# Kernel optimization log

Measured on AMD Instinct MI355X. Metric: run time of the kernel, lower is better.

Reference implementation:

```python
import jax, jax.numpy as jnp
import numpy as np

K_EDE = 10.0   # self.k
T_EDE = 0.1    # self.t
BN_EPS = 1e-5
T_A = 576.0    # 3*3*64, hardcoded in my_bn1/my_bn2


def qfn(x, prec):
    # dorefa-style round quantizer with straight-through gradient
    n = float(2 ** prec - 1)
    return x + jax.lax.stop_gradient(jnp.round(x * n) / n - x)


@jax.custom_vjp
def binary_quantize(x):
    return jnp.sign(x)


def _bq_fwd(x):
    return jnp.sign(x), x


def _bq_bwd(x, g):
    # IR-Net EDE backward: k * t * (1 - tanh(x*t)^2)
    return (K_EDE * T_EDE * (1.0 - jnp.tanh(x * T_EDE) ** 2) * g,)


binary_quantize.defvjp(_bq_fwd, _bq_bwd)


def _clip_T(x):
    T = jnp.maximum(jnp.abs(x.min()), jnp.abs(x.max()))
    return jax.lax.stop_gradient(jnp.clip(T, 1e-10, 255.0))


def quantize_conv_act(x, prec):
    # my_quantize_conv: clamp to [-T, T], scale to [-1,1], qfn (no rescale by T)
    T = _clip_T(x)
    return qfn(jnp.clip(x, -T, T) / T, prec)


def quantize(x, prec):
    # my_quantize: same but rescaled back by T
    T = _clip_T(x)
    return qfn(jnp.clip(x, -T, T) / T, prec) * T


def ir_conv2d(a, w, stride):
    # IR-Net 1w8a IRConv2d: per-out-channel normalize, binarize (sign), power-of-2 scale
    co = w.shape[0]
    wf = w.reshape(co, -1)
    bw = (w - wf.mean(1)[:, None, None, None]) / jnp.std(wf, axis=1, ddof=1)[:, None, None, None]
    sw = jax.lax.stop_gradient(
        2.0 ** jnp.round(jnp.log2(jnp.abs(bw.reshape(co, -1)).mean(1)))
    )[:, None, None, None]
    bw = binary_quantize(bw) * sw
    return jax.lax.conv_general_dilated(
        a, bw, window_strides=(stride, stride), padding=[(1, 1), (1, 1)],
        dimension_numbers=('NCHW', 'OIHW', 'NCHW'))


def bn_as_quantized_affine(x, gamma, beta, mean, var):
    # my_bn1/my_bn2 (eval mode): BN folded into per-channel scale+bias.
    # The original builds a CxC diagonal 1x1 conv; since off-diagonal entries are 0,
    # both the quantization stats (max|.|) and the conv reduce exactly to this
    # per-channel affine, which is the faithful fused form.
    std = jnp.sqrt(var + BN_EPS)
    w = gamma / std
    b = beta - w * mean
    qw = quantize(w, 3)
    qb = quantize(b, 12)
    aq = qfn(x / T_A, 10) * T_A  # my_quantize_activation(input, 10, T_a)
    return aq * qw[None, :, None, None] + qb[None, :, None, None]


def _block(x, w1, w2, g1, b1, m1, v1, g2, b2, m2, v2):
    xq = quantize_conv_act(x, 3)
    out = ir_conv2d(xq, w1, 1)
    out = bn_as_quantized_affine(out, g1, b1, m1, v1) + xq  # identity shortcut
    out = jnp.clip(out, -1.0, 1.0)  # hardtanh
    x1 = quantize_conv_act(out, 3)
    out = ir_conv2d(x1, w2, 1)
    out = bn_as_quantized_affine(out, g2, b2, m2, v2) + x1
    return jnp.clip(out, -1.0, 1.0)


def setup_inputs() -> dict:
    key = jax.random.key(0)
    ks = jax.random.split(key, 11)
    B, C, H, W = 128, 64, 56, 56
    return {
        'x': jax.random.normal(ks[0], (B, C, H, W), jnp.float32),
        'w1': jax.random.normal(ks[1], (C, C, 3, 3), jnp.float32) * 0.1,
        'w2': jax.random.normal(ks[2], (C, C, 3, 3), jnp.float32) * 0.1,
        'g1': jax.random.uniform(ks[3], (C,), jnp.float32, 0.5, 1.5),
        'b1': jax.random.normal(ks[4], (C,), jnp.float32) * 0.1,
        'm1': jax.random.normal(ks[5], (C,), jnp.float32) * 0.1,
        'v1': jax.random.uniform(ks[6], (C,), jnp.float32, 0.5, 1.5),
        'g2': jax.random.uniform(ks[7], (C,), jnp.float32, 0.5, 1.5),
        'b2': jax.random.normal(ks[8], (C,), jnp.float32) * 0.1,
        'm2': jax.random.normal(ks[9], (C,), jnp.float32) * 0.1,
        'v2': jax.random.uniform(ks[10], (C,), jnp.float32, 0.5, 1.5),
    }


def reference(x, w1, w2, g1, b1, m1, v1, g2, b2, m2, v2):
    return _block(x, w1, w2, g1, b1, m1, v1, g2, b2, m2, v2)
```

## Files before the change

kernel.cpp:

```cpp
#include <hip/hip_runtime.h>
#include <stdint.h>

typedef int v4i   __attribute__((ext_vector_type(4)));
typedef int v16i  __attribute__((ext_vector_type(16)));

#define B_    128
#define C_    64
#define H_    56
#define W_    56
#define HW_   3136
#define NELEM (B_*C_*HW_)

#define OFF_K0   0
#define OFF_K1   ((size_t)NELEM)
#define OFF_WB   ((size_t)2*NELEM)
#define OFF_PAR  (OFF_WB + 2*4*9*64*16)
#define OFF_MAX  (OFF_PAR + 384*4)

__device__ __forceinline__ float pw_reduce64(float r) {
    r = __fadd_rn(r, __shfl_xor(r, 1, 64));
    r = __fadd_rn(r, __shfl_xor(r, 2, 64));
    r = __fadd_rn(r, __shfl_xor(r, 4, 64));
    r = __fadd_rn(r, __shfl_xor(r, 8, 64));
    r = __fadd_rn(r, __shfl_xor(r, 16, 64));
    r = __fadd_rn(r, __shfl_xor(r, 32, 64));
    return r;
}

__global__ void k_pre(const float* __restrict__ x, unsigned* __restrict__ maxbits,
                      const float* __restrict__ w1, const float* __restrict__ w2,
                      int8_t* __restrict__ wb, float* __restrict__ par,
                      const float* __restrict__ g1, const float* __restrict__ bb1,
                      const float* __restrict__ mm1, const float* __restrict__ vv1,
                      const float* __restrict__ g2, const float* __restrict__ bb2,
                      const float* __restrict__ mm2, const float* __restrict__ vv2) {
    __shared__ float smax[4];
    const int b = blockIdx.x;
    const int tid = threadIdx.x;
    if (b < 1024) {
        float m = 0.f;
        const int n4 = NELEM / 4;
        for (int i = b * 256 + tid; i < n4; i += 1024 * 256) {
            float4 v = ((const float4*)x)[i];
            m = fmaxf(m, fmaxf(fmaxf(fabsf(v.x), fabsf(v.y)), fmaxf(fabsf(v.z), fabsf(v.w))));
        }
        for (int off = 32; off; off >>= 1) m = fmaxf(m, __shfl_down(m, off, 64));
        if ((tid & 63) == 0) smax[tid >> 6] = m;
        __syncthreads();
        if (tid == 0) {
            float mm = fmaxf(fmaxf(smax[0], smax[1]), fmaxf(smax[2], smax[3]));
            atomicMax(maxbits, __float_as_uint(mm));
        }
    } else if (b < 1056) {
        const int idx = (b - 1024) * 4 + (tid >> 6);
        const int layer = idx >> 6, co = idx & 63;
        const int lane = tid & 63;
        const float* w = (layer ? w2 : w1) + (size_t)co * 576;
        const int base = (lane >> 3) * 72 + (lane & 7);

        float v[9];
#pragma unroll
        for (int i = 0; i < 9; i++) v[i] = w[base + 8 * i];

        float s = v[0];
#pragma unroll
        for (int i = 1; i < 9; i++) s = __fadd_rn(s, v[i]);
        const float mean = __fdiv_rn(pw_reduce64(s), 576.0f);

        float d0 = __fsub_rn(v[0], mean);
        float sq = __fmul_rn(d0, d0);
#pragma unroll
        for (int i = 1; i < 9; i++) {
            float d = __fsub_rn(v[i], mean);
            sq = __fadd_rn(sq, __fmul_rn(d, d));
        }
        const float sig = __fsqrt_rn(__fdiv_rn(pw_reduce64(sq), 575.0f));

        float sa = fabsf(__fdiv_rn(__fsub_rn(v[0], mean), sig));
#pragma unroll
        for (int i = 1; i < 9; i++)
            sa = __fadd_rn(sa, fabsf(__fdiv_rn(__fsub_rn(v[i], mean), sig)));
        const float ma = __fdiv_rn(pw_reduce64(sa), 576.0f);
        const float p  = rintf(log2f(ma));
        if (lane == 0) par[256 + layer * 64 + co] = __fdiv_rn(exp2f(p), 7.0f);

#pragma unroll
        for (int i = 0; i < 9; i++) {
            int ig = base + 8 * i;
            float d = __fsub_rn(v[i], mean);
            int8_t sg = (d > 0.0f) ? (int8_t)1 : ((d < 0.0f) ? (int8_t)-1 : (int8_t)0);
            int ci = ig / 9, tp = ig % 9;
            wb[((((size_t)layer * 4 + (ci >> 4)) * 9 + tp) * 64 + co) * 16 + (ci & 15)] = sg;
        }
    } else {
        if (tid < 128) {
            const int layer = tid >> 6;
            const int c = tid & 63;
            const float* g  = layer ? g2  : g1;
            const float* be = layer ? bb2 : bb1;
            const float* mu = layer ? mm2 : mm1;
            const float* va = layer ? vv2 : vv1;
            const float stdv = __fsqrt_rn(__fadd_rn(va[c], 1e-5f));
            const float w = __fdiv_rn(g[c], stdv);
            const float bb = __fsub_rn(be[c], __fmul_rn(w, mu[c]));
            float aw = fabsf(w), ab = fabsf(bb);
            for (int off = 32; off; off >>= 1) {
                aw = fmaxf(aw, __shfl_xor(aw, off, 64));
                ab = fmaxf(ab, __shfl_xor(ab, off, 64));
            }
            const float Tw = fminf(fmaxf(aw, 1e-10f), 255.0f);
            const float Tb = fminf(fmaxf(ab, 1e-10f), 255.0f);
            {
                float vq = __fdiv_rn(fminf(fmaxf(w, -Tw), Tw), Tw);
                float r  = rintf(__fmul_rn(vq, 7.0f));
                float qf = __fadd_rn(vq, __fsub_rn(__fdiv_rn(r, 7.0f), vq));
                par[layer * 64 + c] = __fmul_rn(qf, Tw);
            }
            {
                float vq = __fdiv_rn(fminf(fmaxf(bb, -Tb), Tb), Tb);
                float r  = rintf(__fmul_rn(vq, 4095.0f));
                float qf = __fadd_rn(vq, __fsub_rn(__fdiv_rn(r, 4095.0f), vq));
                par[128 + layer * 64 + c] = __fmul_rn(qf, Tb);
            }
        }
    }
}

__global__ void k_quant(const float* __restrict__ x, const unsigned* __restrict__ maxbits,
                        int8_t* __restrict__ k8) {
    __shared__ unsigned tile[56 * 17];
    const int n = blockIdx.x / H_;
    const int y = blockIdx.x % H_;
    const float T = fminf(fmaxf(__uint_as_float(*maxbits), 1e-10f), 255.0f);
    const double dinv = 1.0 / (double)T;
    const int t = threadIdx.x;
    if (t < 224) {
        const int cb = t / 14, xb = t % 14;
        const float* src = x + ((size_t)(n * 64 + 4 * cb)) * HW_ + y * 56 + 4 * xb;
        int kq[4][4];
#pragma unroll
        for (int i = 0; i < 4; i++) {
            float4 v = *(const float4*)(src + (size_t)i * HW_);
            const float e[4] = {v.x, v.y, v.z, v.w};
#pragma unroll
            for (int j = 0; j < 4; j++) {
                const float tc = fminf(fmaxf(e[j], -T), T);
                const float u  = (float)((double)tc * dinv);
                kq[i][j] = (int)rintf(__fmul_rn(u, 7.0f));
            }
        }
#pragma unroll
        for (int j = 0; j < 4; j++) {
            const unsigned d = (kq[0][j] & 255) | ((kq[1][j] & 255) << 8) |
                               ((kq[2][j] & 255) << 16) | ((unsigned)(kq[3][j] & 255) << 24);
            tile[(4 * xb + j) * 17 + cb] = d;
        }
    }
    __syncthreads();
    unsigned* dst = (unsigned*)(k8 + ((size_t)(n * 56 + y)) * 56 * 64);
    for (int u = t; u < 896; u += 256)
        dst[u] = tile[(u >> 4) * 17 + (u & 15)];
}

#define EPI_CHAIN(S_, scf_, kc_, qwf_, qbf_, OUT_)                          \
    {   const float Sf_ = (float)(S_);                                      \
        const float convf_ = __fmul_rn(Sf_, scf_);                          \
        const float xb_ = (float)((double)convf_ * (1.0 / 576.0));          \
        const float rr_ = rintf(__fmul_rn(xb_, 1023.0f));                   \
        const float q1_ = (float)((double)rr_ * (1.0 / 1023.0));            \
        const float y1_ = __fadd_rn(xb_, __fsub_rn(q1_, xb_));              \
        const float aq_ = __fmul_rn(y1_, 576.0f);                           \
        const float xqv_ = (float)((double)(kc_) * (1.0 / 7.0));            \
        float vv_ = __fadd_rn(__fadd_rn(__fmul_rn(aq_, qwf_), qbf_), xqv_); \
        OUT_ = fminf(fmaxf(vv_, -1.0f), 1.0f); }

__global__ __launch_bounds__(448, 2) void k_fused(const int8_t* __restrict__ k0,
                                                  const int8_t* __restrict__ wb,
                                                  const float* __restrict__ par,
                                                  float* __restrict__ fout) {
    __shared__ __align__(16) int8_t wsm[2 * 4 * 9 * 64 * 16];
    __shared__ __align__(16) int8_t k0b[4 * 8 * 58 * 16];
    __shared__ __align__(16) int8_t x1b[4 * 8 * 58 * 16];
    const int n = blockIdx.x >> 1;
    const int b = (blockIdx.x & 1) * 28;
    const int tid = threadIdx.x;
    const int wv = tid >> 6, lane = tid & 63;
    const int mbase = wv * 32;
    const int ml = lane & 31;
    const int khalf = lane >> 5;
    const int m = mbase + ml;
    const int ym = m / 56, cm = m % 56;

    for (int u = tid; u < 4608; u += 448)
        *(int4*)(wsm + u * 16) = *(const int4*)(wb + (size_t)u * 16);
    for (int u = tid; u < 1392; u += 448) {
        const int q = u & 3, vv = u >> 2;
        const int rr = vv / 58, xp = vv % 58;
        const int r = b - 2 + rr, xg = xp - 1;
        int4 val = {0, 0, 0, 0};
        if (r >= 0 && r < 56 && xg >= 0 && xg < 56)
            val = *(const int4*)(k0 + (((size_t)(n * 56 + r)) * 56 + xg) * 64 + q * 16);
        *(int4*)(k0b + (((q * 8 + ((r + 2) & 7)) * 58 + xp) << 4)) = val;
    }
    if (tid < 64) {
        const int q = tid & 3, slot = (tid >> 2) & 7, xs = (tid >> 5) & 1;
        *(int4*)(x1b + (((q * 8 + slot) * 58 + xs * 57) << 4)) = (int4){0, 0, 0, 0};
    }
    __syncthreads();

    const float* qw1 = par;       const float* qw2 = par + 64;
    const float* qb1 = par + 128; const float* qb2 = par + 192;
    const float* sc1 = par + 256; const float* sc2 = par + 320;

    int4 pre[3];
#pragma unroll 1
    for (int i = 0; i < 8; ++i) {
        if (i < 7) {
            const int R0 = b + 4 * i + 4;
#pragma unroll
            for (int it = 0; it < 3; ++it) {
                const int u = tid + it * 448;
                int4 val = {0, 0, 0, 0};
                if (u < 928) {
                    const int q = u & 3, vv = u >> 2;
                    const int rr = vv / 58, xp = vv % 58;
                    const int r = R0 + rr, xg = xp - 1;
                    if (r >= 0 && r < 56 && xg >= 0 && xg < 56)
                        val = *(const int4*)(k0 + (((size_t)(n * 56 + r)) * 56 + xg) * 64 + q * 16);
                }
                pre[it] = val;
            }
        }
        const int y1base = b - 1 + 4 * i;
        {
            v16i acc0, acc1;
#pragma unroll
            for (int z = 0; z < 16; z++) { acc0[z] = 0; acc1[z] = 0; }
#pragma unroll
            for (int s = 0; s < 9; s++) {
                const int ky = s / 3, kx = s % 3;
                const int arow = y1base + ym + ky - 1;
                const int aslot = (arow + 2) & 7;
#pragma unroll
                for (int kb = 0; kb < 2; kb++) {
                    const int q = khalf + 2 * kb;
                    v4i a  = *(const v4i*)(k0b + (((q * 8 + aslot) * 58 + cm + kx) << 4));
                    v4i b0 = *(const v4i*)(wsm + (((q * 9 + s) * 64 + ml) << 4));
                    v4i b1 = *(const v4i*)(wsm + (((q * 9 + s) * 64 + 32 + ml) << 4));
                    acc0 = __builtin_amdgcn_mfma_i32_32x32x32_i8(a, b0, acc0, 0, 0, 0);
                    acc1 = __builtin_amdgcn_mfma_i32_32x32x32_i8(a, b1, acc1, 0, 0, 0);
                }
            }
            const int bsh = (ml & 3) * 8;
#pragma unroll
            for (int t = 0; t < 2; t++) {
                const int co = ml + t * 32;
                const float qwf = qw1[co], qbf = qb1[co], scf = sc1[co];
                const int qc = co >> 4, cl = co & 15;
                const int clw = cl & ~3, cb8 = (cl & 3) * 8;
#pragma unroll
                for (int g = 0; g < 4; g++) {
                    const int mb = mbase + 8 * g + 4 * khalf;
                    const int rl = mb / 56, c0 = mb % 56;
                    const int y1g = y1base + rl;
                    const bool vrow = (y1g >= 0) && (y1g <= 55);
                    const bool wen  = (y1g <= b + 28);
                    const int ksl = (y1g + 2) & 7;
                    const int xsl = (y1g + 1) & 7;
                    const int resb = (qc * 8 + ksl) * 58 + c0 + 1;
                    const int outb = (qc * 8 + xsl) * 58 + c0 + 1;
#pragma unroll
                    for (int i4 = 0; i4 < 4; i4++) {
                        const int S = t ? acc1[4 * g + i4] : acc0[4 * g + i4];
                        const unsigned wd = *(const unsigned*)(k0b + ((resb + i4) << 4) + clw);
                        const int kc = (int)(int8_t)(wd >> cb8);
                        float val; EPI_CHAIN(S, scf, kc, qwf, qbf, val);
                        int k2 = (int)rintf(__fmul_rn(val, 7.0f));
                        if (!vrow) k2 = 0;
                        unsigned vp = ((unsigned)(k2 & 255)) << bsh;
                        vp |= (unsigned)__shfl_xor((int)vp, 1, 64);
                        vp |= (unsigned)__shfl_xor((int)vp, 2, 64);
                        if (wen && (ml & 3) == 0)
                            *(unsigned*)(x1b + ((outb + i4) << 4) + clw) = vp;
                    }
                }
            }
        }
        __syncthreads();

        if (i < 7) {
            const int R0 = b + 4 * i + 4;
#pragma unroll
            for (int it = 0; it < 3; ++it) {
                const int u = tid + it * 448;
                if (u < 928) {
                    const int q = u & 3, vv = u >> 2;
                    const int rr = vv / 58, xp = vv % 58;
                    const int r = R0 + rr;
                    *(int4*)(k0b + (((q * 8 + ((r + 2) & 7)) * 58 + xp) << 4)) = pre[it];
                }
            }
        }
        if (i >= 1) {
            const int y2base = b + 4 * (i - 1);
            v16i acc0, acc1;
#pragma unroll
            for (int z = 0; z < 16; z++) { acc0[z] = 0; acc1[z] = 0; }
#pragma unroll
            for (int s = 0; s < 9; s++) {
                const int ky = s / 3, kx = s % 3;
                const int arow = y2base + ym + ky - 1;
                const int aslot = (arow + 1) & 7;
#pragma unroll
                for (int kb = 0; kb < 2; kb++) {
                    const int q = khalf + 2 * kb;
                    v4i a  = *(const v4i*)(x1b + (((q * 8 + aslot) * 58 + cm + kx) << 4));
                    v4i b0 = *(const v4i*)(wsm + 36864 + (((q * 9 + s) * 64 + ml) << 4));
                    v4i b1 = *(const v4i*)(wsm + 36864 + (((q * 9 + s) * 64 + 32 + ml) << 4));
                    acc0 = __builtin_amdgcn_mfma_i32_32x32x32_i8(a, b0, acc0, 0, 0, 0);
                    acc1 = __builtin_amdgcn_mfma_i32_32x32x32_i8(a, b1, acc1, 0, 0, 0);
                }
            }
#pragma unroll
            for (int t = 0; t < 2; t++) {
                const int co = ml + t * 32;
                const float qwf = qw2[co], qbf = qb2[co], scf = sc2[co];
                const int qc = co >> 4, cl = co & 15;
                const int clw = cl & ~3, cb8 = (cl & 3) * 8;
#pragma unroll
                for (int g = 0; g < 4; g++) {
                    const int mb = mbase + 8 * g + 4 * khalf;
                    const int rl = mb / 56, c0 = mb % 56;
                    const int y2g = y2base + rl;
                    const int xsl = (y2g + 1) & 7;
                    const int resb = (qc * 8 + xsl) * 58 + c0 + 1;
                    float vals[4];
#pragma unroll
                    for (int i4 = 0; i4 < 4; i4++) {
                        const int S = t ? acc1[4 * g + i4] : acc0[4 * g + i4];
                        const unsigned wd = *(const unsigned*)(x1b + ((resb + i4) << 4) + clw);
                        const int kc = (int)(int8_t)(wd >> cb8);
                        EPI_CHAIN(S, scf, kc, qwf, qbf, vals[i4]);
                    }
                    float4 o = make_float4(vals[0], vals[1], vals[2], vals[3]);
                    *(float4*)(fout + ((size_t)(n * 64 + co)) * HW_ + y2g * 56 + c0) = o;
                }
            }
        }
        if (i < 7) __syncthreads();
    }
}

extern "C" void kernel_launch(void* const* d_in, const int* in_sizes, int n_in,
                              void* d_out, int out_size, void* d_ws, size_t ws_size,
                              hipStream_t stream) {
    const float* x  = (const float*)d_in[0];
    const float* w1 = (const float*)d_in[1];
    const float* w2 = (const float*)d_in[2];
    const float* g1 = (const float*)d_in[3];
    const float* b1 = (const float*)d_in[4];
    const float* m1 = (const float*)d_in[5];
    const float* v1 = (const float*)d_in[6];
    const float* g2 = (const float*)d_in[7];
    const float* b2 = (const float*)d_in[8];
    const float* m2 = (const float*)d_in[9];
    const float* v2 = (const float*)d_in[10];

    char* ws = (char*)d_ws;
    int8_t*  k0  = (int8_t*)(ws + OFF_K0);
    int8_t*  wbp = (int8_t*)(ws + OFF_WB);
    float*   par = (float*)(ws + OFF_PAR);
    unsigned* mx = (unsigned*)(ws + OFF_MAX);

    hipMemsetAsync(mx, 0, 4, stream);
    k_pre<<<1057, 256, 0, stream>>>(x, mx, w1, w2, wbp, par,
                                    g1, b1, m1, v1, g2, b2, m2, v2);
    k_quant<<<B_ * H_, 256, 0, stream>>>(x, mx, k0);
    k_fused<<<B_ * 2, 448, 0, stream>>>(k0, wbp, par, (float*)d_out);
}
```

Baseline: 313.9 us.

## Split fused block into concurrent conv1 and conv2 wave groups

Doubles the block to 896 threads and gives the first 7 waves conv1 and the second 7 waves conv2, so the two convolutions run concurrently on different row bands instead of one after the other. The x1 ring buffer in LDS grows from 8 to 12 row slots (mod-12 indexing) so that conv2 can trail conv1 by one more stage, and the loop gains an extra iteration. The aim is to overlap the two stages' MFMA and epilogue work and hide latency within a block. In exchange it raises LDS use and the per-block thread count, which may limit occupancy, and it adds a second barrier per iteration. Launch bounds (896,4) also constrain registers.

```diff
diff --git a/kernel.cpp b/kernel.cpp
--- a/kernel.cpp
+++ b/kernel.cpp
@@ -174,26 +174,27 @@
         float vv_ = __fadd_rn(__fadd_rn(__fmul_rn(aq_, qwf_), qbf_), xqv_); \
         OUT_ = fminf(fmaxf(vv_, -1.0f), 1.0f); }
 
-__global__ __launch_bounds__(448, 2) void k_fused(const int8_t* __restrict__ k0,
+__global__ __launch_bounds__(896, 4) void k_fused(const int8_t* __restrict__ k0,
                                                   const int8_t* __restrict__ wb,
                                                   const float* __restrict__ par,
                                                   float* __restrict__ fout) {
     __shared__ __align__(16) int8_t wsm[2 * 4 * 9 * 64 * 16];
     __shared__ __align__(16) int8_t k0b[4 * 8 * 58 * 16];
-    __shared__ __align__(16) int8_t x1b[4 * 8 * 58 * 16];
+    __shared__ __align__(16) int8_t x1b[4 * 12 * 58 * 16];
     const int n = blockIdx.x >> 1;
     const int b = (blockIdx.x & 1) * 28;
     const int tid = threadIdx.x;
     const int wv = tid >> 6, lane = tid & 63;
-    const int mbase = wv * 32;
+    const bool grp1 = (wv < 7);
+    const int mbase = (grp1 ? wv : (wv - 7)) * 32;
     const int ml = lane & 31;
     const int khalf = lane >> 5;
     const int m = mbase + ml;
     const int ym = m / 56, cm = m % 56;
 
-    for (int u = tid; u < 4608; u += 448)
+    for (int u = tid; u < 4608; u += 896)
         *(int4*)(wsm + u * 16) = *(const int4*)(wb + (size_t)u * 16);
-    for (int u = tid; u < 1392; u += 448) {
+    for (int u = tid; u < 1392; u += 896) {
         const int q = u & 3, vv = u >> 2;
         const int rr = vv / 58, xp = vv % 58;
         const int r = b - 2 + rr, xg = xp - 1;
@@ -202,93 +203,147 @@
             val = *(const int4*)(k0 + (((size_t)(n * 56 + r)) * 56 + xg) * 64 + q * 16);
         *(int4*)(k0b + (((q * 8 + ((r + 2) & 7)) * 58 + xp) << 4)) = val;
     }
-    if (tid < 64) {
-        const int q = tid & 3, slot = (tid >> 2) & 7, xs = (tid >> 5) & 1;
-        *(int4*)(x1b + (((q * 8 + slot) * 58 + xs * 57) << 4)) = (int4){0, 0, 0, 0};
+    if (tid < 96) {
+        const int q = tid & 3, rest = tid >> 2;
+        const int slot = rest % 12, xs = rest / 12;
+        *(int4*)(x1b + (((q * 12 + slot) * 58 + xs * 57) << 4)) = (int4){0, 0, 0, 0};
     }
     __syncthreads();
 
-    const float* qw1 = par;       const float* qw2 = par + 64;
-    const float* qb1 = par + 128; const float* qb2 = par + 192;
-    const float* sc1 = par + 256; const float* sc2 = par + 320;
+    float qwf_[2], qbf_[2], scf_[2];
+#pragma unroll
+    for (int t = 0; t < 2; t++) {
+        const int co = ml + t * 32;
+        if (grp1) { qwf_[t] = par[co];      qbf_[t] = par[128 + co]; scf_[t] = par[256 + co]; }
+        else      { qwf_[t] = par[64 + co]; qbf_[t] = par[192 + co]; scf_[t] = par[320 + co]; }
+    }
 
     int4 pre[3];
 #pragma unroll 1
-    for (int i = 0; i < 8; ++i) {
-        if (i < 7) {
-            const int R0 = b + 4 * i + 4;
-#pragma unroll
-            for (int it = 0; it < 3; ++it) {
-                const int u = tid + it * 448;
-                int4 val = {0, 0, 0, 0};
-                if (u < 928) {
-                    const int q = u & 3, vv = u >> 2;
-                    const int rr = vv / 58, xp = vv % 58;
-                    const int r = R0 + rr, xg = xp - 1;
-                    if (r >= 0 && r < 56 && xg >= 0 && xg < 56)
-                        val = *(const int4*)(k0 + (((size_t)(n * 56 + r)) * 56 + xg) * 64 + q * 16);
-                }
-                pre[it] = val;
-            }
-        }
-        const int y1base = b - 1 + 4 * i;
-        {
-            v16i acc0, acc1;
-#pragma unroll
-            for (int z = 0; z < 16; z++) { acc0[z] = 0; acc1[z] = 0; }
-#pragma unroll
-            for (int s = 0; s < 9; s++) {
-                const int ky = s / 3, kx = s % 3;
-                const int arow = y1base + ym + ky - 1;
-                const int aslot = (arow + 2) & 7;
-#pragma unroll
-                for (int kb = 0; kb < 2; kb++) {
-                    const int q = khalf + 2 * kb;
-                    v4i a  = *(const v4i*)(k0b + (((q * 8 + aslot) * 58 + cm + kx) << 4));
-                    v4i b0 = *(const v4i*)(wsm + (((q * 9 + s) * 64 + ml) << 4));
-                    v4i b1 = *(const v4i*)(wsm + (((q * 9 + s) * 64 + 32 + ml) << 4));
-                    acc0 = __builtin_amdgcn_mfma_i32_32x32x32_i8(a, b0, acc0, 0, 0, 0);
-                    acc1 = __builtin_amdgcn_mfma_i32_32x32x32_i8(a, b1, acc1, 0, 0, 0);
-                }
-            }
-            const int bsh = (ml & 3) * 8;
-#pragma unroll
-            for (int t = 0; t < 2; t++) {
-                const int co = ml + t * 32;
-                const float qwf = qw1[co], qbf = qb1[co], scf = sc1[co];
-                const int qc = co >> 4, cl = co & 15;
-                const int clw = cl & ~3, cb8 = (cl & 3) * 8;
-#pragma unroll
-                for (int g = 0; g < 4; g++) {
-                    const int mb = mbase + 8 * g + 4 * khalf;
-                    const int rl = mb / 56, c0 = mb % 56;
-                    const int y1g = y1base + rl;
-                    const bool vrow = (y1g >= 0) && (y1g <= 55);
-                    const bool wen  = (y1g <= b + 28);
-                    const int ksl = (y1g + 2) & 7;
-                    const int xsl = (y1g + 1) & 7;
-                    const int resb = (qc * 8 + ksl) * 58 + c0 + 1;
-                    const int outb = (qc * 8 + xsl) * 58 + c0 + 1;
-#pragma unroll
-                    for (int i4 = 0; i4 < 4; i4++) {
-                        const int S = t ? acc1[4 * g + i4] : acc0[4 * g + i4];
-                        const unsigned wd = *(const unsigned*)(k0b + ((resb + i4) << 4) + clw);
-                        const int kc = (int)(int8_t)(wd >> cb8);
-                        float val; EPI_CHAIN(S, scf, kc, qwf, qbf, val);
-                        int k2 = (int)rintf(__fmul_rn(val, 7.0f));
-                        if (!vrow) k2 = 0;
-                        unsigned vp = ((unsigned)(k2 & 255)) << bsh;
-                        vp |= (unsigned)__shfl_xor((int)vp, 1, 64);
-                        vp |= (unsigned)__shfl_xor((int)vp, 2, 64);
-                        if (wen && (ml & 3) == 0)
-                            *(unsigned*)(x1b + ((outb + i4) << 4) + clw) = vp;
+    for (int i = 0; i < 9; ++i) {
+        if (grp1) {
+            if (i < 7) {
+                const int R0 = b + 4 * i + 4;
+#pragma unroll
+                for (int it = 0; it < 3; ++it) {
+                    const int u = tid + it * 448;
+                    int4 val = {0, 0, 0, 0};
+                    if (u < 928) {
+                        const int q = u & 3, vv = u >> 2;
+                        const int rr = vv / 58, xp = vv % 58;
+                        const int r = R0 + rr, xg = xp - 1;
+                        if (r >= 0 && r < 56 && xg >= 0 && xg < 56)
+                            val = *(const int4*)(k0 + (((size_t)(n * 56 + r)) * 56 + xg) * 64 + q * 16);
+                    }
+                    pre[it] = val;
+                }
+            }
+            if (i < 8) {
+                const int y1base = b - 1 + 4 * i;
+                v16i acc0, acc1;
+#pragma unroll
+                for (int z = 0; z < 16; z++) { acc0[z] = 0; acc1[z] = 0; }
+#pragma unroll
+                for (int s = 0; s < 9; s++) {
+                    const int ky = s / 3, kx = s % 3;
+                    const int arow = y1base + ym + ky - 1;
+                    const int aslot = (arow + 2) & 7;
+#pragma unroll
+                    for (int kb = 0; kb < 2; kb++) {
+                        const int q = khalf + 2 * kb;
+                        v4i a  = *(const v4i*)(k0b + (((q * 8 + aslot) * 58 + cm + kx) << 4));
+                        v4i b0 = *(const v4i*)(wsm + (((q * 9 + s) * 64 + ml) << 4));
+                        v4i b1 = *(const v4i*)(wsm + (((q * 9 + s) * 64 + 32 + ml) << 4));
+                        acc0 = __builtin_amdgcn_mfma_i32_32x32x32_i8(a, b0, acc0, 0, 0, 0);
+                        acc1 = __builtin_amdgcn_mfma_i32_32x32x32_i8(a, b1, acc1, 0, 0, 0);
+                    }
+                }
+                const int bsh = (ml & 3) * 8;
+#pragma unroll
+                for (int t = 0; t < 2; t++) {
+                    const int co = ml + t * 32;
+                    const float qwf = qwf_[t], qbf = qbf_[t], scf = scf_[t];
+                    const int qc = co >> 4, cl = co & 15;
+                    const int clw = cl & ~3, cb8 = (cl & 3) * 8;
+#pragma unroll
+                    for (int g = 0; g < 4; g++) {
+                        const int mb = mbase + 8 * g + 4 * khalf;
+                        const int rl = mb / 56, c0 = mb % 56;
+                        const int y1g = y1base + rl;
+                        const bool vrow = (y1g >= 0) && (y1g <= 55);
+                        const bool wen  = (y1g <= b + 28);
+                        const int ksl = (y1g + 2) & 7;
+                        const int xsl = (y1g + 12) % 12;
+                        const int resb = (qc * 8 + ksl) * 58 + c0 + 1;
+                        const int outb = (qc * 12 + xsl) * 58 + c0 + 1;
+#pragma unroll
+                        for (int i4 = 0; i4 < 4; i4++) {
+                            const int S = t ? acc1[4 * g + i4] : acc0[4 * g + i4];
+                            const unsigned wd = *(const unsigned*)(k0b + ((resb + i4) << 4) + clw);
+                            const int kc = (int)(int8_t)(wd >> cb8);
+                            float val; EPI_CHAIN(S, scf, kc, qwf, qbf, val);
+                            int k2 = (int)rintf(__fmul_rn(val, 7.0f));
+                            if (!vrow) k2 = 0;
+                            unsigned vp = ((unsigned)(k2 & 255)) << bsh;
+                            vp |= (unsigned)__shfl_xor((int)vp, 1, 64);
+                            vp |= (unsigned)__shfl_xor((int)vp, 2, 64);
+                            if (wen && (ml & 3) == 0)
+                                *(unsigned*)(x1b + ((outb + i4) << 4) + clw) = vp;
+                        }
+                    }
+                }
+            }
+        } else {
+            if (i >= 2) {
+                const int y2base = b + 4 * (i - 2);
+                v16i acc0, acc1;
+#pragma unroll
+                for (int z = 0; z < 16; z++) { acc0[z] = 0; acc1[z] = 0; }
+#pragma unroll
+                for (int s = 0; s < 9; s++) {
+                    const int ky = s / 3, kx = s % 3;
+                    const int arow = y2base + ym + ky - 1;
+                    const int aslot = (arow + 12) % 12;
+#pragma unroll
+                    for (int kb = 0; kb < 2; kb++) {
+                        const int q = khalf + 2 * kb;
+                        v4i a  = *(const v4i*)(x1b + (((q * 12 + aslot) * 58 + cm + kx) << 4));
+                        v4i b0 = *(const v4i*)(wsm + 36864 + (((q * 9 + s) * 64 + ml) << 4));
+                        v4i b1 = *(const v4i*)(wsm + 36864 + (((q * 9 + s) * 64 + 32 + ml) << 4));
+                        acc0 = __builtin_amdgcn_mfma_i32_32x32x32_i8(a, b0, acc0, 0, 0, 0);
+                        acc1 = __builtin_amdgcn_mfma_i32_32x32x32_i8(a, b1, acc1, 0, 0, 0);
+                    }
+                }
+#pragma unroll
+                for (int t = 0; t < 2; t++) {
+                    const int co = ml + t * 32;
+                    const float qwf = qwf_[t], qbf = qbf_[t], scf = scf_[t];
+                    const int qc = co >> 4, cl = co & 15;
+                    const int clw = cl & ~3, cb8 = (cl & 3) * 8;
+#pragma unroll
+                    for (int g = 0; g < 4; g++) {
+                        const int mb = mbase + 8 * g + 4 * khalf;
+                        const int rl = mb / 56, c0 = mb % 56;
+                        const int y2g = y2base + rl;
+                        const int xsl = (y2g + 12) % 12;
+                        const int resb = (qc * 12 + xsl) * 58 + c0 + 1;
+                        float vals[4];
+#pragma unroll
+                        for (int i4 = 0; i4 < 4; i4++) {
+                            const int S = t ? acc1[4 * g + i4] : acc0[4 * g + i4];
+                            const unsigned wd = *(const unsigned*)(x1b + ((resb + i4) << 4) + clw);
+                            const int kc = (int)(int8_t)(wd >> cb8);
+                            EPI_CHAIN(S, scf, kc, qwf, qbf, vals[i4]);
+                        }
+                        float4 o = make_float4(vals[0], vals[1], vals[2], vals[3]);
+                        *(float4*)(fout + ((size_t)(n * 64 + co)) * HW_ + y2g * 56 + c0) = o;
                     }
                 }
             }
         }
         __syncthreads();
 
-        if (i < 7) {
+        if (grp1 && i < 7) {
             const int R0 = b + 4 * i + 4;
 #pragma unroll
             for (int it = 0; it < 3; ++it) {
@@ -301,53 +356,7 @@
                 }
             }
         }
-        if (i >= 1) {
-            const int y2base = b + 4 * (i - 1);
-            v16i acc0, acc1;
-#pragma unroll
-            for (int z = 0; z < 16; z++) { acc0[z] = 0; acc1[z] = 0; }
-#pragma unroll
-            for (int s = 0; s < 9; s++) {
-                const int ky = s / 3, kx = s % 3;
-                const int arow = y2base + ym + ky - 1;
-                const int aslot = (arow + 1) & 7;
-#pragma unroll
-                for (int kb = 0; kb < 2; kb++) {
-                    const int q = khalf + 2 * kb;
-                    v4i a  = *(const v4i*)(x1b + (((q * 8 + aslot) * 58 + cm + kx) << 4));
-                    v4i b0 = *(const v4i*)(wsm + 36864 + (((q * 9 + s) * 64 + ml) << 4));
-                    v4i b1 = *(const v4i*)(wsm + 36864 + (((q * 9 + s) * 64 + 32 + ml) << 4));
-                    acc0 = __builtin_amdgcn_mfma_i32_32x32x32_i8(a, b0, acc0, 0, 0, 0);
-                    acc1 = __builtin_amdgcn_mfma_i32_32x32x32_i8(a, b1, acc1, 0, 0, 0);
-                }
-            }
-#pragma unroll
-            for (int t = 0; t < 2; t++) {
-                const int co = ml + t * 32;
-                const float qwf = qw2[co], qbf = qb2[co], scf = sc2[co];
-                const int qc = co >> 4, cl = co & 15;
-                const int clw = cl & ~3, cb8 = (cl & 3) * 8;
-#pragma unroll
-                for (int g = 0; g < 4; g++) {
-                    const int mb = mbase + 8 * g + 4 * khalf;
-                    const int rl = mb / 56, c0 = mb % 56;
-                    const int y2g = y2base + rl;
-                    const int xsl = (y2g + 1) & 7;
-                    const int resb = (qc * 8 + xsl) * 58 + c0 + 1;
-                    float vals[4];
-#pragma unroll
-                    for (int i4 = 0; i4 < 4; i4++) {
-                        const int S = t ? acc1[4 * g + i4] : acc0[4 * g + i4];
-                        const unsigned wd = *(const unsigned*)(x1b + ((resb + i4) << 4) + clw);
-                        const int kc = (int)(int8_t)(wd >> cb8);
-                        EPI_CHAIN(S, scf, kc, qwf, qbf, vals[i4]);
-                    }
-                    float4 o = make_float4(vals[0], vals[1], vals[2], vals[3]);
-                    *(float4*)(fout + ((size_t)(n * 64 + co)) * HW_ + y2g * 56 + c0) = o;
-                }
-            }
-        }
-        if (i < 7) __syncthreads();
+        __syncthreads();
     }
 }
 
@@ -376,5 +385,5 @@
     k_pre<<<1057, 256, 0, stream>>>(x, mx, w1, w2, wbp, par,
                                     g1, b1, m1, v1, g2, b2, m2, v2);
     k_quant<<<B_ * H_, 256, 0, stream>>>(x, mx, k0);
-    k_fused<<<B_ * 2, 448, 0, stream>>>(k0, wbp, par, (float*)d_out);
-}
+    k_fused<<<B_ * 2, 896, 0, stream>>>(k0, wbp, par, (float*)d_out);
+}
```

New measurement: 292.1 us. 6.9% less time.
